# Kernel optimization log

Measured on AMD Instinct MI355X. Metric: run time of the kernel, lower is better.

## Reference

```python
import jax, jax.numpy as jnp
import numpy as np

CONTEXT = 3  # config['context']
B, H, W = 8, 256, 256
NBR = 2 * CONTEXT  # number of similarity branches


def _conv(x, w, b):
    # x: [N, Cin, H, W], w: [Cout, Cin, kh, kw], SAME padding, stride 1
    y = jax.lax.conv_general_dilated(x, w, (1, 1), 'SAME',
                                     dimension_numbers=('NCHW', 'OIHW', 'NCHW'))
    return y + b[None, :, None, None]


def setup_inputs() -> dict:
    key = jax.random.key(0)
    ks = jax.random.split(key, 5)
    x = jax.random.normal(ks[0], (B, 2 * CONTEXT + 1, H, W), dtype=jnp.float32)
    # kaiming-ish scaled inits
    W1 = jax.random.normal(ks[1], (NBR, 64, 2, 3, 3), dtype=jnp.float32) * (2.0 / (64 * 9)) ** 0.5
    b1 = jnp.zeros((NBR, 64), dtype=jnp.float32)
    W2 = jax.random.normal(ks[2], (NBR, 1, 64, 1, 1), dtype=jnp.float32) * (2.0 / 1) ** 0.5 * 0.1
    b2 = jnp.zeros((NBR, 1), dtype=jnp.float32)
    Wm = jax.random.normal(ks[3], (7, 7, 3, 3), dtype=jnp.float32) * (2.0 / (7 * 9)) ** 0.5
    bm = jnp.zeros((7,), dtype=jnp.float32)
    return {'x': x, 'W1': W1, 'b1': b1, 'W2': W2, 'b2': b2, 'Wm': Wm, 'bm': bm}


def reference(x, W1, b1, W2, b2, Wm, bm):
    # mode == 'context' path just returns x; this implements the main path.
    base = x[:, CONTEXT:CONTEXT + 1]                                  # [B,1,H,W]
    checks = jnp.concatenate([x[:, :CONTEXT], x[:, CONTEXT + 1:]], axis=1)  # [B,6,H,W]
    check_e = checks[:, :, None]                                      # [B,6,1,H,W]
    base_e = jnp.broadcast_to(base[:, None], check_e.shape)           # [B,6,1,H,W]
    # channel order: pre-frames -> (base, check); post-frames -> (check, base)
    ch0 = jnp.concatenate([base_e[:, :CONTEXT], check_e[:, CONTEXT:]], axis=2 - 2 + 2)  # placeholder
    ch0 = jnp.concatenate([base_e[:, :CONTEXT], check_e[:, CONTEXT:]], axis=1)
    ch1 = jnp.concatenate([check_e[:, :CONTEXT], base_e[:, CONTEXT:]], axis=1)
    pairs = jnp.concatenate([ch0, ch1], axis=2)                       # [B,6,2,H,W]
    pairs = jnp.swapaxes(pairs, 0, 1)                                 # [6,B,2,H,W]

    def branch(pair, w1, bb1, w2, bb2):
        h = jax.nn.relu(_conv(pair, w1, bb1))                         # [B,64,H,W]
        return jax.nn.sigmoid(_conv(h, w2, bb2))                      # [B,1,H,W]

    sims = jax.vmap(branch)(pairs, W1, b1, W2, b2)                    # [6,B,1,H,W]
    weighted = sims[:, :, 0] * jnp.swapaxes(checks, 0, 1)             # [6,B,H,W]
    weighted = jnp.swapaxes(weighted, 0, 1)                           # [B,6,H,W]
    combined = jnp.concatenate([weighted[:, :CONTEXT], base, weighted[:, CONTEXT:]], axis=1)  # [B,7,H,W]
    return _conv(combined, Wm, bm)                                    # [B,7,H,W]
```

## Files before the change

kernel.cpp:

```cpp
#include <hip/hip_runtime.h>
#include <math.h>

#define Bn 8
#define Hn 256
#define Wn 256
#define HW (Hn * Wn)
#define ROWS 8
#define RP 264
#define ZW (20 * RP)

typedef __attribute__((ext_vector_type(8))) short bf16x8;
typedef __attribute__((ext_vector_type(4))) float f32x4;
typedef __attribute__((ext_vector_type(2))) float f32x2;

__device__ __forceinline__ unsigned int pk_bits(unsigned int lo,
                                                unsigned int hi) {
  return __builtin_amdgcn_perm(hi, lo, 0x07060302u);
}
__device__ __forceinline__ unsigned int pk_bf16(float lo, float hi) {
  return pk_bits(__float_as_uint(lo), __float_as_uint(hi));
}

__device__ __constant__ const int T0c[8] = {0, 1, 2, 9, 10, 11, 3, 4};
__device__ __constant__ const int T1c[8] = {6, 7, 8, 15, 16, 17, 12, 13};
__device__ __constant__ const int T2c[8] = {5, 14, -1, -1, -1, -1, -1, -1};

__global__ __launch_bounds__(256) void sim_kernel(
    const float* __restrict__ x,
    const float* __restrict__ W1,
    const float* __restrict__ b1,
    const float* __restrict__ W2,
    const float* __restrict__ b2,
    float* __restrict__ comb)
{
  __shared__ float rowsF[20 * RP + 64];
  __shared__ uint4 wq[4][64];

  int bi = blockIdx.x;
  int n  = bi >> 8;
  int b  = (bi >> 5) & 7;
  int h0 = (bi & 31) * ROWS;
  int cc = (n < 3) ? n : n + 1;
  int t = threadIdx.x;

  const float* xb     = x + (size_t)b * 7 * HW;
  const float* basep  = xb + 3 * HW;
  const float* checkp = xb + (size_t)cc * HW;

  {
    int f = t >> 6, qq = (t >> 4) & 3, m = t & 15;
    int bsrc = (n < 3) ? 0 : 1;
    const float* wch = W1 + ((size_t)(n * 64 + 16 * f + m)) * 18;
    unsigned int kv[4];
#pragma unroll
    for (int jj = 0; jj < 4; ++jj) {
      int ja = 2 * jj, jb = 2 * jj + 1;
      int ta = (qq == 0) ? T0c[ja] : (qq == 1) ? T1c[ja]
               : (qq == 2) ? T2c[ja] : -1;
      int tb = (qq == 0) ? T0c[jb] : (qq == 1) ? T1c[jb]
               : (qq == 2) ? T2c[jb] : -1;
      float va = 0.f, vb = 0.f;
      if (ta >= 0) {
        int pl = ta / 9, rem = ta - pl * 9;
        va = wch[(pl ? 1 - bsrc : bsrc) * 9 + rem];
      }
      if (tb >= 0) {
        int pl = tb / 9, rem = tb - pl * 9;
        vb = wch[(pl ? 1 - bsrc : bsrc) * 9 + rem];
      }
      kv[jj] = pk_bf16(va, vb);
    }
    wq[f][(qq << 4) + m] = make_uint4(kv[0], kv[1], kv[2], kv[3]);
  }

  int lane = t & 63, wvid = t >> 6;
  int q = lane >> 4, m_ = lane & 15;
  f32x2 w2A[4], w2B[4];
  f32x4 b1vv[4];
#pragma unroll
  for (int f = 0; f < 4; ++f) {
    float4 tw = *(const float4*)&W2[n * 64 + 16 * f + 4 * q];
    float4 tb = *(const float4*)&b1[n * 64 + 16 * f + 4 * q];
    w2A[f][0] = tw.x; w2A[f][1] = tw.y;
    w2B[f][0] = tw.z; w2B[f][1] = tw.w;
    b1vv[f][0] = tb.x; b1vv[f][1] = tb.y;
    b1vv[f][2] = tb.z; b1vv[f][3] = tb.w;
  }
  float bb = b2[n];

  {
    int col = (t & 63) << 2;
#pragma unroll
    for (int it = 0; it < 5; ++it) {
      int rf = it * 4 + (t >> 6);
      int pl = (rf >= 10) ? 1 : 0;
      int j  = rf - pl * 10;
      int hh = h0 - 1 + j;
      const float* src = pl ? checkp : basep;
      float4 val = make_float4(0.f, 0.f, 0.f, 0.f);
      if ((unsigned)hh < (unsigned)Hn)
        val = *(const float4*)(src + hh * Wn + col);
      *(float4*)&rowsF[rf * RP + 4 + col] = val;
    }
    if (t < 20) {
      rowsF[t * RP + 3] = 0.f;
      rowsF[t * RP + 260] = 0.f;
    }
    if (t >= 192) rowsF[ZW + (t - 192)] = 0.f;
  }

  const unsigned int* rowsU = (const unsigned int*)rowsF;
  unsigned int addr[8], step[8];
#pragma unroll
  for (int jh = 0; jh < 8; ++jh) {
    int tap = (q == 0) ? T0c[jh] : (q == 1) ? T1c[jh]
              : (q == 2) ? T2c[jh] : -1;
    if (tap >= 0) {
      int pl = tap / 9, rem = tap - pl * 9;
      int rr = rem / 3, dx = rem - rr * 3;
      addr[jh] = (pl * 10 + rr) * RP + 3 + dx + wvid * 64 + m_;
      step[jh] = (unsigned)RP;
    } else {
      addr[jh] = (unsigned)ZW;
      step[jh] = 0u;
    }
  }

  __syncthreads();

  bf16x8 afrag[4];
#pragma unroll
  for (int f = 0; f < 4; ++f) afrag[f] = *(const bf16x8*)&wq[f][lane];

  float* combcc = comb + ((size_t)b * 7 + cc) * HW;
  int pxs = wvid * 64 + lane;

#pragma unroll 1
  for (int r = 0; r < ROWS; ++r) {
    int h = h0 + r;

    float g[4];
#pragma unroll
    for (int half = 0; half < 2; ++half) {
      unsigned int dlo[8], dhi[8];
#pragma unroll
      for (int jh = 0; jh < 8; ++jh) {
        dlo[jh] = rowsU[addr[jh] + half * 32];
        dhi[jh] = rowsU[addr[jh] + half * 32 + 16];
      }
#pragma unroll
      for (int j = 0; j < 2; ++j) {
        const unsigned int* d = j ? dhi : dlo;
        union { unsigned int u[4]; bf16x8 v; } bu;
#pragma unroll
        for (int jj = 0; jj < 4; ++jj)
          bu.u[jj] = pk_bits(d[2 * jj], d[2 * jj + 1]);

        f32x4 acc[4];
#pragma unroll
        for (int f = 0; f < 4; ++f)
          acc[f] = __builtin_amdgcn_mfma_f32_16x16x32_bf16(afrag[f], bu.v,
                                                           b1vv[f], 0, 0, 0);

        f32x2 sA = {0.f, 0.f}, sB = {0.f, 0.f};
#pragma unroll
        for (int f = 0; f < 4; ++f) {
          f32x2 a01, a23;
          a01[0] = acc[f][0]; a01[1] = acc[f][1];
          a23[0] = acc[f][2]; a23[1] = acc[f][3];
          a01 = __builtin_elementwise_max(a01, (f32x2)0.f);
          a23 = __builtin_elementwise_max(a23, (f32x2)0.f);
          sA += w2A[f] * a01;
          sB += w2B[f] * a23;
        }
        float sp = (sA[0] + sB[0]) + (sA[1] + sB[1]);
        sp += __shfl_xor(sp, 16, 64);
        sp += __shfl_xor(sp, 32, 64);
        sp += bb;

        float e = __builtin_amdgcn_exp2f(sp * -1.442695041f);
        g[2 * half + j] = __builtin_amdgcn_rcpf(1.f + e);
      }
    }

    int hi = lane >> 4;
    float gsel = (hi == 0) ? g[0] : (hi == 1) ? g[1] : (hi == 2) ? g[2] : g[3];
    float ccv = rowsF[(10 + r + 1) * RP + 4 + pxs];
    combcc[h * Wn + pxs] = gsel * ccv;

#pragma unroll
    for (int jh = 0; jh < 8; ++jh) addr[jh] += step[jh];
  }
}

__global__ __launch_bounds__(512) void mix_kernel(
    const float* __restrict__ comb,
    const float* __restrict__ x,
    const float* __restrict__ Wm,
    const float* __restrict__ bm,
    float* __restrict__ out)
{
  __shared__ float mr[42 * RP];

  int bi = blockIdx.x;
  int b  = bi >> 6;
  int h0 = (bi & 63) << 2;
  int t = threadIdx.x;

  for (int u = t; u < 42 * 64; u += 512) {
    int rf = u >> 6;
    int col = (u & 63) << 2;
    int ic = rf / 6, j = rf - ic * 6;
    int hh = h0 - 1 + j;
    const float* src = (ic == 3) ? (x + ((size_t)b * 7 + 3) * HW)
                                 : (comb + ((size_t)b * 7 + ic) * HW);
    float4 v = make_float4(0.f, 0.f, 0.f, 0.f);
    if ((unsigned)hh < (unsigned)Hn)
      v = *(const float4*)(src + hh * Wn + col);
    *(float4*)&mr[rf * RP + 4 + col] = v;
  }
  if (t < 42) {
    mr[t * RP + 3] = 0.f;
    mr[t * RP + 260] = 0.f;
  }
  __syncthreads();

  int r   = t >> 7;
  int px0 = (t & 127) << 1;
  int h   = h0 + r;

  float acc[7][2];
#pragma unroll
  for (int oc = 0; oc < 7; ++oc) {
    float bv = bm[oc];
    acc[oc][0] = bv;
    acc[oc][1] = bv;
  }

#pragma unroll 1
  for (int ic = 0; ic < 7; ++ic) {
    float w[3][4];
#pragma unroll
    for (int dy = 0; dy < 3; ++dy) {
      const float* rp = &mr[(ic * 6 + r + dy) * RP + 3 + px0];
      w[dy][0] = rp[0]; w[dy][1] = rp[1];
      w[dy][2] = rp[2]; w[dy][3] = rp[3];
    }
    const float* wp = Wm + ic * 9;
#pragma unroll
    for (int oc = 0; oc < 7; ++oc) {
      const float* wo = wp + oc * 63;
#pragma unroll
      for (int dy = 0; dy < 3; ++dy)
#pragma unroll
        for (int dx = 0; dx < 3; ++dx) {
          float wvv = wo[dy * 3 + dx];
          acc[oc][0] = fmaf(wvv, w[dy][0 + dx], acc[oc][0]);
          acc[oc][1] = fmaf(wvv, w[dy][1 + dx], acc[oc][1]);
        }
    }
  }

  float* ob = out + (size_t)b * 7 * HW + h * Wn + px0;
#pragma unroll
  for (int oc = 0; oc < 7; ++oc)
    *(float2*)(ob + (size_t)oc * HW) = make_float2(acc[oc][0], acc[oc][1]);
}

extern "C" void kernel_launch(void* const* d_in, const int* in_sizes, int n_in,
                              void* d_out, int out_size, void* d_ws, size_t ws_size,
                              hipStream_t stream) {
  const float* x  = (const float*)d_in[0];
  const float* W1 = (const float*)d_in[1];
  const float* b1 = (const float*)d_in[2];
  const float* W2 = (const float*)d_in[3];
  const float* b2 = (const float*)d_in[4];
  const float* Wm = (const float*)d_in[5];
  const float* bm = (const float*)d_in[6];
  float* out  = (float*)d_out;
  float* comb = (float*)d_ws;

  sim_kernel<<<6 * 8 * (Hn / ROWS), 256, 0, stream>>>(x, W1, b1, W2, b2, comb);
  mix_kernel<<<8 * (Hn / 4), 512, 0, stream>>>(comb, x, Wm, bm, out);
}
```

Before: 118.2 us.

## Software-pipeline LDS loads and interleave MFMA pairs in sim kernel

```diff
diff --git a/kernel.cpp b/kernel.cpp
--- a/kernel.cpp
+++ b/kernel.cpp
@@ -25,7 +25,7 @@
 __device__ __constant__ const int T1c[8] = {6, 7, 8, 15, 16, 17, 12, 13};
 __device__ __constant__ const int T2c[8] = {5, 14, -1, -1, -1, -1, -1, -1};
 
-__global__ __launch_bounds__(256) void sim_kernel(
+__global__ __launch_bounds__(256, 4) void sim_kernel(
     const float* __restrict__ x,
     const float* __restrict__ W1,
     const float* __restrict__ b1,
@@ -110,7 +110,7 @@
   }
 
   const unsigned int* rowsU = (const unsigned int*)rowsF;
-  unsigned int addr[8], step[8];
+  unsigned int addr[8];
 #pragma unroll
   for (int jh = 0; jh < 8; ++jh) {
     int tap = (q == 0) ? T0c[jh] : (q == 1) ? T1c[jh]
@@ -119,12 +119,13 @@
       int pl = tap / 9, rem = tap - pl * 9;
       int rr = rem / 3, dx = rem - rr * 3;
       addr[jh] = (pl * 10 + rr) * RP + 3 + dx + wvid * 64 + m_;
-      step[jh] = (unsigned)RP;
     } else {
       addr[jh] = (unsigned)ZW;
-      step[jh] = 0u;
-    }
-  }
+    }
+  }
+  unsigned int stepA = (q <= 2) ? (unsigned)RP : 0u;
+  unsigned int stepB = (q < 2) ? (unsigned)RP : 0u;
+  int bpaddr = ((lane ^ 32) << 2);
 
   __syncthreads();
 
@@ -135,61 +136,91 @@
   float* combcc = comb + ((size_t)b * 7 + cc) * HW;
   int pxs = wvid * 64 + lane;
 
+  auto compute2 = [&](const unsigned int* dbuf, float& gA, float& gB) {
+    union { unsigned int u[4]; bf16x8 v; } p0, p1;
+#pragma unroll
+    for (int jj = 0; jj < 4; ++jj) {
+      p0.u[jj] = pk_bits(dbuf[2 * jj], dbuf[2 * jj + 1]);
+      p1.u[jj] = pk_bits(dbuf[8 + 2 * jj], dbuf[8 + 2 * jj + 1]);
+    }
+    f32x4 acc0[4], acc1[4];
+#pragma unroll
+    for (int f = 0; f < 4; ++f) {
+      acc0[f] = __builtin_amdgcn_mfma_f32_16x16x32_bf16(afrag[f], p0.v,
+                                                        b1vv[f], 0, 0, 0);
+      acc1[f] = __builtin_amdgcn_mfma_f32_16x16x32_bf16(afrag[f], p1.v,
+                                                        b1vv[f], 0, 0, 0);
+    }
+    f32x2 sA0 = {0.f, 0.f}, sB0 = {0.f, 0.f};
+    f32x2 sA1 = {0.f, 0.f}, sB1 = {0.f, 0.f};
+#pragma unroll
+    for (int f = 0; f < 4; ++f) {
+      f32x2 a01, a23, c01, c23;
+      a01[0] = acc0[f][0]; a01[1] = acc0[f][1];
+      a23[0] = acc0[f][2]; a23[1] = acc0[f][3];
+      c01[0] = acc1[f][0]; c01[1] = acc1[f][1];
+      c23[0] = acc1[f][2]; c23[1] = acc1[f][3];
+      a01 = __builtin_elementwise_max(a01, (f32x2)0.f);
+      a23 = __builtin_elementwise_max(a23, (f32x2)0.f);
+      c01 = __builtin_elementwise_max(c01, (f32x2)0.f);
+      c23 = __builtin_elementwise_max(c23, (f32x2)0.f);
+      sA0 += w2A[f] * a01;
+      sB0 += w2B[f] * a23;
+      sA1 += w2A[f] * c01;
+      sB1 += w2B[f] * c23;
+    }
+    float sp0 = (sA0[0] + sB0[0]) + (sA0[1] + sB0[1]);
+    float sp1 = (sA1[0] + sB1[0]) + (sA1[1] + sB1[1]);
+    sp0 += __int_as_float(
+        __builtin_amdgcn_ds_swizzle(__float_as_int(sp0), 0x401F));
+    sp1 += __int_as_float(
+        __builtin_amdgcn_ds_swizzle(__float_as_int(sp1), 0x401F));
+    sp0 += __int_as_float(
+        __builtin_amdgcn_ds_bpermute(bpaddr, __float_as_int(sp0)));
+    sp1 += __int_as_float(
+        __builtin_amdgcn_ds_bpermute(bpaddr, __float_as_int(sp1)));
+    sp0 += bb;
+    sp1 += bb;
+    float e0 = __builtin_amdgcn_exp2f(sp0 * -1.442695041f);
+    float e1 = __builtin_amdgcn_exp2f(sp1 * -1.442695041f);
+    gA = __builtin_amdgcn_rcpf(1.f + e0);
+    gB = __builtin_amdgcn_rcpf(1.f + e1);
+  };
+
+  unsigned int bufA[16], bufB[16];
+#pragma unroll
+  for (int jh = 0; jh < 8; ++jh) {
+    bufA[jh]     = rowsU[addr[jh]];
+    bufA[jh + 8] = rowsU[addr[jh] + 16];
+  }
+
 #pragma unroll 1
   for (int r = 0; r < ROWS; ++r) {
-    int h = h0 + r;
-
-    float g[4];
-#pragma unroll
-    for (int half = 0; half < 2; ++half) {
-      unsigned int dlo[8], dhi[8];
+    float ccv = rowsF[(10 + r + 1) * RP + 4 + pxs];
+
+#pragma unroll
+    for (int jh = 0; jh < 8; ++jh) {
+      bufB[jh]     = rowsU[addr[jh] + 32];
+      bufB[jh + 8] = rowsU[addr[jh] + 48];
+    }
+
+    float g0, g1, g2, g3;
+    compute2(bufA, g0, g1);
+
+    if (r < ROWS - 1) {
 #pragma unroll
       for (int jh = 0; jh < 8; ++jh) {
-        dlo[jh] = rowsU[addr[jh] + half * 32];
-        dhi[jh] = rowsU[addr[jh] + half * 32 + 16];
+        addr[jh] += (jh < 2) ? stepA : stepB;
+        bufA[jh]     = rowsU[addr[jh]];
+        bufA[jh + 8] = rowsU[addr[jh] + 16];
       }
-#pragma unroll
-      for (int j = 0; j < 2; ++j) {
-        const unsigned int* d = j ? dhi : dlo;
-        union { unsigned int u[4]; bf16x8 v; } bu;
-#pragma unroll
-        for (int jj = 0; jj < 4; ++jj)
-          bu.u[jj] = pk_bits(d[2 * jj], d[2 * jj + 1]);
-
-        f32x4 acc[4];
-#pragma unroll
-        for (int f = 0; f < 4; ++f)
-          acc[f] = __builtin_amdgcn_mfma_f32_16x16x32_bf16(afrag[f], bu.v,
-                                                           b1vv[f], 0, 0, 0);
-
-        f32x2 sA = {0.f, 0.f}, sB = {0.f, 0.f};
-#pragma unroll
-        for (int f = 0; f < 4; ++f) {
-          f32x2 a01, a23;
-          a01[0] = acc[f][0]; a01[1] = acc[f][1];
-          a23[0] = acc[f][2]; a23[1] = acc[f][3];
-          a01 = __builtin_elementwise_max(a01, (f32x2)0.f);
-          a23 = __builtin_elementwise_max(a23, (f32x2)0.f);
-          sA += w2A[f] * a01;
-          sB += w2B[f] * a23;
-        }
-        float sp = (sA[0] + sB[0]) + (sA[1] + sB[1]);
-        sp += __shfl_xor(sp, 16, 64);
-        sp += __shfl_xor(sp, 32, 64);
-        sp += bb;
-
-        float e = __builtin_amdgcn_exp2f(sp * -1.442695041f);
-        g[2 * half + j] = __builtin_amdgcn_rcpf(1.f + e);
-      }
-    }
+    }
+
+    compute2(bufB, g2, g3);
 
     int hi = lane >> 4;
-    float gsel = (hi == 0) ? g[0] : (hi == 1) ? g[1] : (hi == 2) ? g[2] : g[3];
-    float ccv = rowsF[(10 + r + 1) * RP + 4 + pxs];
-    combcc[h * Wn + pxs] = gsel * ccv;
-
-#pragma unroll
-    for (int jh = 0; jh < 8; ++jh) addr[jh] += step[jh];
+    float gsel = (hi == 0) ? g0 : (hi == 1) ? g1 : (hi == 2) ? g2 : g3;
+    combcc[(h0 + r) * Wn + pxs] = gsel * ccv;
   }
 }
 
```

New measurement: 116.5 us. Within noise of the previous version (-1.5%).
